# Kernel optimization log

Hardware: AMD Instinct MI355X
Metric: run time of the kernel (lower is better)

The kernel has to match this reference:

```python
import jax, jax.numpy as jnp
import numpy as np

# Hardcoded module dims (BClassifier: L=500, D=128, K=1; rehearsal_label=[0,1] => 2 classes)
L = 500
D = 128
NUM_CLASSES = 2
BUFFER_SIZE = 512
PER_CLS = BUFFER_SIZE // NUM_CLASSES  # 256
FEAT = 1024
B = 32
N = 4096
TEMP = 0.5
EPS = 1e-8  # torch cosine_similarity eps


def setup_inputs() -> dict:
    key = jax.random.key(0)
    ks = jax.random.split(key, 12)
    s = 0.02
    return {
        "x": jax.random.normal(ks[0], (B, N, FEAT), jnp.float32),
        "y": jax.random.randint(ks[1], (B,), 0, NUM_CLASSES),
        "W1": jax.random.normal(ks[2], (FEAT, L), jnp.float32) * s,
        "b1": jnp.zeros((L,), jnp.float32),
        "Wa": jax.random.normal(ks[3], (L, D), jnp.float32) * s,
        "ba": jnp.zeros((D,), jnp.float32),
        "Va": jax.random.normal(ks[4], (D, 1), jnp.float32) * s,
        "bv": jnp.zeros((1,), jnp.float32),
        "Wc": jax.random.normal(ks[5], (L, NUM_CLASSES), jnp.float32) * s,
        "bc": jnp.zeros((NUM_CLASSES,), jnp.float32),
        "rehearsal": jax.random.uniform(ks[6], (NUM_CLASSES, PER_CLS, L), jnp.float32),
    }


def _l2norm(v, axis=-1, keepdims=True):
    return jnp.maximum(jnp.linalg.norm(v, axis=axis, keepdims=keepdims), EPS)


def reference(x, y, W1, b1, Wa, ba, Va, bv, Wc, bc, rehearsal):
    # --- attention MIL pooling ---
    H = jax.nn.relu(jnp.einsum("bnf,fl->bnl", x, W1) + b1)          # [B,N,L]
    a = jax.nn.relu(jnp.einsum("bnl,ld->bnd", H, Wa) + ba) @ Va + bv  # [B,N,1]
    A = jax.nn.softmax(a[..., 0], axis=-1)                            # [B,N]
    bag_feat = jnp.einsum("bn,bnl->bl", A, H)                         # [B,L]
    logits_mlp = bag_feat @ Wc + bc                                   # [B,C]

    # --- buffer_update: contrastive loss + reg term ---
    cls_means = jnp.mean(rehearsal, axis=1)                           # [C,L]
    sim = bag_feat @ cls_means.T                                      # [B,C]
    pos = jnp.take_along_axis(sim, y[:, None], axis=1)                # [B,1]
    neg = jnp.take_along_axis(sim, (1 - y)[:, None], axis=1)          # [B,1] (C==2)
    logits = jnp.concatenate([pos, neg], axis=1)
    loss = -jnp.mean(jax.nn.log_softmax(logits / TEMP, axis=1)[:, 0])

    cm_n = cls_means / _l2norm(cls_means)                             # [C,L]
    cc = 1.0 + cm_n @ cm_n.T                                          # [C,C]
    reg = (jnp.sum(cc) - jnp.trace(cc)) / 2.0

    # --- sequential rehearsal scatter update ---
    reh_n = rehearsal / _l2norm(rehearsal)                            # [C,P,L]
    cls_dists = jnp.einsum("cl,cpl->cp", cm_n, reh_n)                 # [C,P]
    bag_n = bag_feat / _l2norm(bag_feat)                              # [B,L]

    def step(carry, inp):
        reh, dists = carry
        xi, xin, ci = inp
        d = jnp.dot(cm_n[ci], xin)                 # cos(cls_means[ci], x_i)
        row = dists[ci]
        idx = jnp.argmin(row)
        mv = row[idx]
        cond = d > mv
        reh = reh.at[ci, idx].set(jnp.where(cond, xi, reh[ci, idx]))
        dists = dists.at[ci, idx].set(jnp.where(cond, d, mv))
        return (reh, dists), None

    (new_rehearsal, _), _ = jax.lax.scan(step, (rehearsal, cls_dists), (bag_feat, bag_n, y))

    return logits_mlp, loss, reg, new_rehearsal
```

## Files before the change

### kernel.cpp

```cpp
#include <hip/hip_runtime.h>


#define EPSF 1e-8f

typedef float v4f __attribute__((ext_vector_type(4)));
typedef short v8s __attribute__((ext_vector_type(8)));

__device__ __forceinline__ unsigned short f2bf(float f) {
  unsigned u = __float_as_uint(f);
  u = (u + 0x7fffu + ((u >> 16) & 1u)) >> 16;
  return (unsigned short)u;
}
__device__ __forceinline__ float bf2f(unsigned short b) {
  return __uint_as_float(((unsigned)b) << 16);
}
__device__ __forceinline__ unsigned pk(float a, float b) {
  return __builtin_amdgcn_perm(__float_as_uint(b), __float_as_uint(a), 0x07060302u);
}
__device__ __forceinline__ void gll16(const void* g, void* l) {
  __builtin_amdgcn_global_load_lds((const __attribute__((address_space(1))) void*)g,
                                   (__attribute__((address_space(3))) void*)l, 16, 0, 0);
}

__global__ void k0_w1t(const float* __restrict__ W1, unsigned short* __restrict__ W1T) {
  int idx = blockIdx.x * 256 + threadIdx.x;
  int n = idx >> 10, k = idx & 1023;
  float v = (n < 500) ? W1[k * 500 + n] : 0.f;
  W1T[idx] = f2bf(v);
}
__global__ void k0_wat(const float* __restrict__ Wa, unsigned short* __restrict__ WaT) {
  int idx = blockIdx.x * 256 + threadIdx.x;
  int d = idx >> 9, l = idx & 511;
  float v = (l < 500) ? Wa[l * 128 + d] : 0.f;
  WaT[idx] = f2bf(v);
}

__global__ __launch_bounds__(256) void k1_gemm1(const float* __restrict__ x,
    const unsigned short* __restrict__ W1T, const float* __restrict__ b1,
    unsigned short* __restrict__ H) {
  __shared__ float As[128 * 64];
  __shared__ unsigned short Bs[128 * 64];
  int bid = blockIdx.x;
  int x8 = bid & 7, j = bid >> 3;
  int mb = x8 * 128 + (j >> 2);
  int n0 = (j & 3) * 128;
  size_t m0 = (size_t)mb * 128;
  int tid = threadIdx.x;
  int lane = tid & 63, wv = tid >> 6;
  int wm = (wv >> 1) * 64, wn = (wv & 1) * 64;
  int l15 = lane & 15, quad = lane >> 4, m7 = l15 & 7;
  v4f acc[4][4];
  for (int i = 0; i < 4; i++)
    for (int jj = 0; jj < 4; jj++) acc[i][jj] = (v4f)(0.f);

  for (int kt = 0; kt < 1024; kt += 64) {
    const float* gA = x + m0 * 1024 + kt;
    const unsigned short* gB = W1T + (size_t)n0 * 1024 + kt;
#pragma unroll
    for (int p = 0; p < 8; p++) {
      int ci = p * 256 + tid;
      int r = ci >> 4, pc = ci & 15;
      int c = pc ^ (r & 7);
      gll16(gA + (size_t)r * 1024 + c * 4, As + ci * 4);
    }
#pragma unroll
    for (int p = 0; p < 4; p++) {
      int ci = p * 256 + tid;
      int r = ci >> 3, pc = ci & 7;
      int c = pc ^ (r & 7);
      gll16(gB + (size_t)r * 1024 + c * 8, Bs + ci * 8);
    }
    __syncthreads();
#pragma unroll
    for (int kk = 0; kk < 64; kk += 32) {
      v8s af[4], bf[4];
      int c0 = (kk >> 2) + 2 * quad;
      int cb = (kk >> 3) + quad;
#pragma unroll
      for (int mi = 0; mi < 4; mi++) {
        const float* rowp = As + (wm + mi * 16 + l15) * 64;
        v4f lo = *(const v4f*)(rowp + ((c0 ^ m7) << 2));
        v4f hi = *(const v4f*)(rowp + (((c0 + 1) ^ m7) << 2));
        union { unsigned u[4]; v8s v; } t;
        t.u[0] = pk(lo.x, lo.y); t.u[1] = pk(lo.z, lo.w);
        t.u[2] = pk(hi.x, hi.y); t.u[3] = pk(hi.z, hi.w);
        af[mi] = t.v;
      }
#pragma unroll
      for (int ni = 0; ni < 4; ni++)
        bf[ni] = *(const v8s*)(Bs + (wn + ni * 16 + l15) * 64 + ((cb ^ m7) << 3));
#pragma unroll
      for (int mi = 0; mi < 4; mi++)
#pragma unroll
        for (int ni = 0; ni < 4; ni++)
          acc[mi][ni] = __builtin_amdgcn_mfma_f32_16x16x32_bf16(af[mi], bf[ni], acc[mi][ni], 0, 0, 0);
    }
    __syncthreads();
  }
#pragma unroll
  for (int mi = 0; mi < 4; mi++) {
#pragma unroll
    for (int ni = 0; ni < 4; ni++) {
      int col = n0 + wn + ni * 16 + l15;
      float bias = (col < 500) ? b1[col] : 0.f;
#pragma unroll
      for (int r = 0; r < 4; r++) {
        size_t row = m0 + wm + mi * 16 + quad * 4 + r;
        float v = (col < 500) ? fmaxf(acc[mi][ni][r] + bias, 0.f) : 0.f;
        H[row * 512 + col] = f2bf(v);
      }
    }
  }
}

__global__ __launch_bounds__(256) void k2_attn(const unsigned short* __restrict__ H,
    const unsigned short* __restrict__ WaT, const float* __restrict__ ba,
    const float* __restrict__ Va, const float* __restrict__ bv,
    float* __restrict__ aout) {
  __shared__ unsigned short Hs[128 * 64];
  __shared__ unsigned short Ws[128 * 64];
  size_t m0 = (size_t)blockIdx.x * 128;
  int tid = threadIdx.x;
  int lane = tid & 63, wv = tid >> 6;
  int wm = wv * 32;
  int l15 = lane & 15, quad = lane >> 4, m7 = l15 & 7;
  v4f acc[2][8];
  for (int i = 0; i < 2; i++)
    for (int jj = 0; jj < 8; jj++) acc[i][jj] = (v4f)(0.f);

  for (int kt = 0; kt < 512; kt += 64) {
    const unsigned short* gH = H + m0 * 512 + kt;
    const unsigned short* gW = WaT + kt;
#pragma unroll
    for (int p = 0; p < 4; p++) {
      int ci = p * 256 + tid;
      int r = ci >> 3, pc = ci & 7;
      int c = pc ^ (r & 7);
      gll16(gH + (size_t)r * 512 + c * 8, Hs + ci * 8);
    }
#pragma unroll
    for (int p = 0; p < 4; p++) {
      int ci = p * 256 + tid;
      int r = ci >> 3, pc = ci & 7;
      int c = pc ^ (r & 7);
      gll16(gW + (size_t)r * 512 + c * 8, Ws + ci * 8);
    }
    __syncthreads();
#pragma unroll
    for (int kk = 0; kk < 64; kk += 32) {
      v8s af[2], bf[8];
      int cb = (kk >> 3) + quad;
#pragma unroll
      for (int mi = 0; mi < 2; mi++)
        af[mi] = *(const v8s*)(Hs + (wm + mi * 16 + l15) * 64 + ((cb ^ m7) << 3));
#pragma unroll
      for (int ni = 0; ni < 8; ni++)
        bf[ni] = *(const v8s*)(Ws + (ni * 16 + l15) * 64 + ((cb ^ m7) << 3));
#pragma unroll
      for (int mi = 0; mi < 2; mi++)
#pragma unroll
        for (int ni = 0; ni < 8; ni++)
          acc[mi][ni] = __builtin_amdgcn_mfma_f32_16x16x32_bf16(af[mi], bf[ni], acc[mi][ni], 0, 0, 0);
    }
    __syncthreads();
  }
  float bav[8], vav[8];
#pragma unroll
  for (int ni = 0; ni < 8; ni++) {
    int n = ni * 16 + l15;
    bav[ni] = ba[n];
    vav[ni] = Va[n];
  }
  float bv0 = bv[0];
#pragma unroll
  for (int mi = 0; mi < 2; mi++) {
#pragma unroll
    for (int r = 0; r < 4; r++) {
      float s = 0.f;
#pragma unroll
      for (int ni = 0; ni < 8; ni++) s += fmaxf(acc[mi][ni][r] + bav[ni], 0.f) * vav[ni];
      s += __shfl_xor(s, 1); s += __shfl_xor(s, 2);
      s += __shfl_xor(s, 4); s += __shfl_xor(s, 8);
      if (l15 == 0) aout[m0 + wm + mi * 16 + quad * 4 + r] = s + bv0;
    }
  }
}

__global__ void k3_softmax(float* __restrict__ a) {
  __shared__ float red[256];
  int b = blockIdx.x, tid = threadIdx.x;
  float* row = a + b * 4096;
  float m = -1e30f;
  for (int i = tid; i < 4096; i += 256) m = fmaxf(m, row[i]);
  red[tid] = m; __syncthreads();
  for (int s = 128; s > 0; s >>= 1) { if (tid < s) red[tid] = fmaxf(red[tid], red[tid + s]); __syncthreads(); }
  m = red[0]; __syncthreads();
  float sum = 0.f;
  for (int i = tid; i < 4096; i += 256) { float e = expf(row[i] - m); row[i] = e; sum += e; }
  red[tid] = sum; __syncthreads();
  for (int s = 128; s > 0; s >>= 1) { if (tid < s) red[tid] += red[tid + s]; __syncthreads(); }
  float inv = 1.f / red[0];
  for (int i = tid; i < 4096; i += 256) row[i] *= inv;
}

__global__ void k4_bag(const unsigned short* __restrict__ H, const float* __restrict__ A,
                       float* __restrict__ bag) {
  int bid = blockIdx.x;
  int b = bid >> 4, ch = bid & 15;
  int tid = threadIdx.x;
  size_t base = ((size_t)b * 4096 + ch * 256) * 512;
  const float* Ab = A + b * 4096 + ch * 256;
  float s0 = 0.f, s1 = 0.f;
  for (int n = 0; n < 256; n += 4) {
#pragma unroll
    for (int jj = 0; jj < 4; jj++) {
      float w = Ab[n + jj];
      unsigned hv = *(const unsigned*)(H + base + (size_t)(n + jj) * 512 + tid * 2);
      s0 += w * bf2f((unsigned short)(hv & 0xffffu));
      s1 += w * bf2f((unsigned short)(hv >> 16));
    }
  }
  atomicAdd(&bag[b * 512 + tid * 2], s0);
  atomicAdd(&bag[b * 512 + tid * 2 + 1], s1);
}

__global__ void k5_copy(const float* __restrict__ reh, float* __restrict__ out) {
  int idx = blockIdx.x * 256 + threadIdx.x;
  if (idx < 256000) out[66 + idx] = reh[idx];
}

__global__ void k5_means(const float* __restrict__ reh, float* __restrict__ cm) {
  int c = blockIdx.x, tid = threadIdx.x;
  const float* base = reh + c * 128000;
  float s0 = 0.f, s1 = 0.f;
  for (int q = 0; q < 256; q++) {
    const float* row = base + q * 500;
    s0 += row[tid];
    if (tid + 256 < 500) s1 += row[tid + 256];
  }
  cm[c * 512 + tid] = s0 * (1.f / 256.f);
  int l2 = tid + 256;
  cm[c * 512 + l2] = (l2 < 500) ? s1 * (1.f / 256.f) : 0.f;
}

__global__ void k5_cmnorm(const float* __restrict__ cm, float* __restrict__ cmn) {
  __shared__ float red[256];
  int c = blockIdx.x, tid = threadIdx.x;
  float v = 0.f;
  for (int l = tid; l < 512; l += 256) { float xx = cm[c * 512 + l]; v += xx * xx; }
  red[tid] = v; __syncthreads();
  for (int s = 128; s > 0; s >>= 1) { if (tid < s) red[tid] += red[tid + s]; __syncthreads(); }
  if (tid == 0) cmn[c] = sqrtf(red[0]);
}

__global__ void k5_dists(const float* __restrict__ reh, const float* __restrict__ cm,
                         const float* __restrict__ cmn, float* __restrict__ dists) {
  int bid = blockIdx.x;
  int c = bid >> 8, p = bid & 255;
  int lane = threadIdx.x;
  const float* row = reh + (c * 256 + p) * 500;
  const float* cmr = cm + c * 512;
  float dot = 0.f, n2 = 0.f;
  for (int l = lane; l < 500; l += 64) { float r = row[l]; dot += r * cmr[l]; n2 += r * r; }
#pragma unroll
  for (int m = 32; m > 0; m >>= 1) { dot += __shfl_xor(dot, m); n2 += __shfl_xor(n2, m); }
  if (lane == 0)
    dists[c * 256 + p] = dot / (fmaxf(cmn[c], EPSF) * fmaxf(sqrtf(n2), EPSF));
}

__global__ __launch_bounds__(256) void k5_head(const float* __restrict__ bag,
    const float* __restrict__ cm, const float* __restrict__ cmn,
    const float* __restrict__ distsIn, const int* __restrict__ y,
    const float* __restrict__ Wc, const float* __restrict__ bc,
    float* __restrict__ out) {
  __shared__ float simL[32][2], logitL[32][2], bagn[32];
  __shared__ int ownS[512];
  __shared__ float dot01S;
  int tid = threadIdx.x;
  int lane = tid & 63, wv = tid >> 6;
  for (int j = 0; j < 8; j++) {
    int b = wv * 8 + j;
    const float* br = bag + b * 512;
    float s0 = 0, s1 = 0, w0 = 0, w1 = 0, n2 = 0;
    for (int l = lane; l < 500; l += 64) {
      float v = br[l];
      s0 += v * cm[l]; s1 += v * cm[512 + l];
      w0 += v * Wc[l * 2]; w1 += v * Wc[l * 2 + 1];
      n2 += v * v;
    }
#pragma unroll
    for (int m = 32; m > 0; m >>= 1) {
      s0 += __shfl_xor(s0, m); s1 += __shfl_xor(s1, m);
      w0 += __shfl_xor(w0, m); w1 += __shfl_xor(w1, m);
      n2 += __shfl_xor(n2, m);
    }
    if (lane == 0) {
      simL[b][0] = s0; simL[b][1] = s1;
      logitL[b][0] = w0 + bc[0]; logitL[b][1] = w1 + bc[1];
      bagn[b] = sqrtf(n2);
    }
  }
  if (wv == 1) {
    float d = 0.f;
    for (int l = lane; l < 500; l += 64) d += cm[l] * cm[512 + l];
#pragma unroll
    for (int m = 32; m > 0; m >>= 1) d += __shfl_xor(d, m);
    if (lane == 0) dot01S = d;
  }
  __syncthreads();
  if (tid < 64) out[tid] = logitL[tid >> 1][tid & 1];
  if (tid == 64) {
    float acc = 0.f;
    for (int b = 0; b < 32; b++) {
      int yb = y[b];
      float p = simL[b][yb] * 2.0f;
      float ng = simL[b][1 - yb] * 2.0f;
      float mx = fmaxf(p, ng);
      float lse = mx + logf(expf(p - mx) + expf(ng - mx));
      acc += p - lse;
    }
    out[64] = -acc / 32.f;
    out[65] = 1.f + dot01S / (fmaxf(cmn[0], EPSF) * fmaxf(cmn[1], EPSF));
  }
  if (wv == 0) {
    float dreg[8]; int oreg[8];
#pragma unroll
    for (int j = 0; j < 8; j++) { dreg[j] = distsIn[j * 64 + lane]; oreg[j] = -1; }
    for (int i = 0; i < 32; i++) {
      int ci = y[i];
      int jb = ci * 4;
      float v = dreg[jb]; int p = lane;
#pragma unroll
      for (int jj = 1; jj < 4; jj++) {
        float nv = dreg[jb + jj]; int np = jj * 64 + lane;
        if (nv < v || (nv == v && np < p)) { v = nv; p = np; }
      }
#pragma unroll
      for (int s = 1; s < 64; s <<= 1) {
        float ov = __shfl_xor(v, s); int op = __shfl_xor(p, s);
        if (ov < v || (ov == v && op < p)) { v = ov; p = op; }
      }
      float d = simL[i][ci] / (fmaxf(cmn[ci], EPSF) * fmaxf(bagn[i], EPSF));
      if (d > v && (p & 63) == lane) {
        int jj = jb + (p >> 6);
        dreg[jj] = d; oreg[jj] = i;
      }
    }
#pragma unroll
    for (int j = 0; j < 8; j++) ownS[j * 64 + lane] = oreg[j];
  }
  __syncthreads();
  for (int s = 0; s < 512; s++) {
    int o = ownS[s];
    if (o >= 0)
      for (int l = tid; l < 500; l += 256) out[66 + s * 500 + l] = bag[o * 512 + l];
  }
}

extern "C" void kernel_launch(void* const* d_in, const int* in_sizes, int n_in,
                              void* d_out, int out_size, void* d_ws, size_t ws_size,
                              hipStream_t stream) {
  const float* x  = (const float*)d_in[0];
  const int*   y  = (const int*)d_in[1];
  const float* W1 = (const float*)d_in[2];
  const float* b1 = (const float*)d_in[3];
  const float* Wa = (const float*)d_in[4];
  const float* ba = (const float*)d_in[5];
  const float* Va = (const float*)d_in[6];
  const float* bv = (const float*)d_in[7];
  const float* Wc = (const float*)d_in[8];
  const float* bc = (const float*)d_in[9];
  const float* reh = (const float*)d_in[10];
  float* out = (float*)d_out;

  char* ws = (char*)d_ws;
  unsigned short* H   = (unsigned short*)ws;
  float*          a   = (float*)(ws + 134217728);
  unsigned short* W1T = (unsigned short*)(ws + 134742016);
  unsigned short* WaT = (unsigned short*)(ws + 135790592);
  float*          bag = (float*)(ws + 135921664);
  float*          cm  = (float*)(ws + 135987200);
  float*          cmn = (float*)(ws + 135991296);
  float*          dst = (float*)(ws + 135991552);

  hipMemsetAsync(bag, 0, 65536, stream);
  k0_w1t<<<2048, 256, 0, stream>>>(W1, W1T);
  k0_wat<<<256, 256, 0, stream>>>(Wa, WaT);
  k1_gemm1<<<4096, 256, 0, stream>>>(x, W1T, b1, H);
  k2_attn<<<1024, 256, 0, stream>>>(H, WaT, ba, Va, bv, a);
  k3_softmax<<<32, 256, 0, stream>>>(a);
  k4_bag<<<512, 256, 0, stream>>>(H, a, bag);
  k5_copy<<<1001, 256, 0, stream>>>(reh, out);
  k5_means<<<2, 256, 0, stream>>>(reh, cm);
  k5_cmnorm<<<2, 256, 0, stream>>>(cm, cmn);
  k5_dists<<<512, 64, 0, stream>>>(reh, cm, cmn, dst);
  k5_head<<<1, 256, 0, stream>>>(bag, cm, cmn, dst, y, Wc, bc, out);
}
```

Baseline: 1.080 ms.

## Widen GEMM1 tile to full N so each x row block is read once

GEMM1 now has each 512-thread block compute a 128x512 output tile covering all of N, instead of four 128x128 tiles that each reloaded the same fp32 rows of x. The x tile is loaded through registers, converted to bf16 once and written to swizzled LDS, replacing the direct global-to-LDS fp32 copy followed by per-fragment conversion. This cuts global reads of x by 4x, the dominant traffic, at the cost of 128 accumulator registers per thread, a larger B tile in LDS, and a synchronous register load path instead of async LDS loads.

Result: faster. 1.038 ms (-3.9%).

```diff
diff --git a/kernel.cpp b/kernel.cpp
--- a/kernel.cpp
+++ b/kernel.cpp
@@ -35,64 +35,60 @@
   WaT[idx] = f2bf(v);
 }
 
-__global__ __launch_bounds__(256) void k1_gemm1(const float* __restrict__ x,
+__global__ __launch_bounds__(512, 2) void k1_gemm1(const float* __restrict__ x,
     const unsigned short* __restrict__ W1T, const float* __restrict__ b1,
     unsigned short* __restrict__ H) {
-  __shared__ float As[128 * 64];
-  __shared__ unsigned short Bs[128 * 64];
-  int bid = blockIdx.x;
-  int x8 = bid & 7, j = bid >> 3;
-  int mb = x8 * 128 + (j >> 2);
-  int n0 = (j & 3) * 128;
-  size_t m0 = (size_t)mb * 128;
+  __shared__ unsigned short As[128 * 64];
+  __shared__ unsigned short Bs[512 * 64];
   int tid = threadIdx.x;
   int lane = tid & 63, wv = tid >> 6;
-  int wm = (wv >> 1) * 64, wn = (wv & 1) * 64;
-  int l15 = lane & 15, quad = lane >> 4, m7 = l15 & 7;
-  v4f acc[4][4];
+  int wm = (wv & 1) * 64, wn = (wv >> 1) * 128;
+  int l15 = lane & 15, quad = lane >> 4;
+  size_t m0 = (size_t)blockIdx.x * 128;
+  v4f acc[4][8];
+#pragma unroll
   for (int i = 0; i < 4; i++)
-    for (int jj = 0; jj < 4; jj++) acc[i][jj] = (v4f)(0.f);
+#pragma unroll
+    for (int j = 0; j < 8; j++) acc[i][j] = (v4f)(0.f);
 
   for (int kt = 0; kt < 1024; kt += 64) {
     const float* gA = x + m0 * 1024 + kt;
-    const unsigned short* gB = W1T + (size_t)n0 * 1024 + kt;
+    const unsigned short* gB = W1T + kt;
+#pragma unroll
+    for (int p = 0; p < 4; p++) {
+      int ci = p * 512 + tid;
+      int r = ci >> 4, c4 = ci & 15;
+      v4f v = *(const v4f*)(gA + (size_t)r * 1024 + c4 * 4);
+      unsigned u0 = pk(v.x, v.y), u1 = pk(v.z, v.w);
+      int c8 = c4 >> 1, half = c4 & 1;
+      unsigned* dst = (unsigned*)(As + r * 64 + (((c8 ^ (r & 7)) << 3) | (half << 2)));
+      dst[0] = u0; dst[1] = u1;
+    }
 #pragma unroll
     for (int p = 0; p < 8; p++) {
-      int ci = p * 256 + tid;
-      int r = ci >> 4, pc = ci & 15;
-      int c = pc ^ (r & 7);
-      gll16(gA + (size_t)r * 1024 + c * 4, As + ci * 4);
-    }
-#pragma unroll
-    for (int p = 0; p < 4; p++) {
-      int ci = p * 256 + tid;
-      int r = ci >> 3, pc = ci & 7;
-      int c = pc ^ (r & 7);
+      int ci = p * 512 + tid;
+      int r = ci >> 3, c = (ci & 7) ^ (r & 7);
       gll16(gB + (size_t)r * 1024 + c * 8, Bs + ci * 8);
     }
     __syncthreads();
 #pragma unroll
     for (int kk = 0; kk < 64; kk += 32) {
-      v8s af[4], bf[4];
-      int c0 = (kk >> 2) + 2 * quad;
+      v8s af[4], bf[8];
       int cb = (kk >> 3) + quad;
 #pragma unroll
       for (int mi = 0; mi < 4; mi++) {
-        const float* rowp = As + (wm + mi * 16 + l15) * 64;
-        v4f lo = *(const v4f*)(rowp + ((c0 ^ m7) << 2));
-        v4f hi = *(const v4f*)(rowp + (((c0 + 1) ^ m7) << 2));
-        union { unsigned u[4]; v8s v; } t;
-        t.u[0] = pk(lo.x, lo.y); t.u[1] = pk(lo.z, lo.w);
-        t.u[2] = pk(hi.x, hi.y); t.u[3] = pk(hi.z, hi.w);
-        af[mi] = t.v;
-      }
-#pragma unroll
-      for (int ni = 0; ni < 4; ni++)
-        bf[ni] = *(const v8s*)(Bs + (wn + ni * 16 + l15) * 64 + ((cb ^ m7) << 3));
+        int r = wm + mi * 16 + l15;
+        af[mi] = *(const v8s*)(As + r * 64 + ((cb ^ (r & 7)) << 3));
+      }
+#pragma unroll
+      for (int ni = 0; ni < 8; ni++) {
+        int r = wn + ni * 16 + l15;
+        bf[ni] = *(const v8s*)(Bs + r * 64 + ((cb ^ (r & 7)) << 3));
+      }
 #pragma unroll
       for (int mi = 0; mi < 4; mi++)
 #pragma unroll
-        for (int ni = 0; ni < 4; ni++)
+        for (int ni = 0; ni < 8; ni++)
           acc[mi][ni] = __builtin_amdgcn_mfma_f32_16x16x32_bf16(af[mi], bf[ni], acc[mi][ni], 0, 0, 0);
     }
     __syncthreads();
@@ -100,8 +96,8 @@
 #pragma unroll
   for (int mi = 0; mi < 4; mi++) {
 #pragma unroll
-    for (int ni = 0; ni < 4; ni++) {
-      int col = n0 + wn + ni * 16 + l15;
+    for (int ni = 0; ni < 8; ni++) {
+      int col = wn + ni * 16 + l15;
       float bias = (col < 500) ? b1[col] : 0.f;
 #pragma unroll
       for (int r = 0; r < 4; r++) {
@@ -386,7 +382,7 @@
   hipMemsetAsync(bag, 0, 65536, stream);
   k0_w1t<<<2048, 256, 0, stream>>>(W1, W1T);
   k0_wat<<<256, 256, 0, stream>>>(Wa, WaT);
-  k1_gemm1<<<4096, 256, 0, stream>>>(x, W1T, b1, H);
+  k1_gemm1<<<1024, 512, 0, stream>>>(x, W1T, b1, H);
   k2_attn<<<1024, 256, 0, stream>>>(H, WaT, ba, Va, bv, a);
   k3_softmax<<<32, 256, 0, stream>>>(a);
   k4_bag<<<512, 256, 0, stream>>>(H, a, bag);
```
